# Optimization experiments

Measured on AMD Instinct MI355X. Metric: run time of the kernel, lower is better.

## Reference

```python
import jax, jax.numpy as jnp
import numpy as np

B, N, E, D, M, T, P, HS, HN, C, NH = 64, 1024, 512, 1024, 16, 12, 2048, 2048, 64, 4, 8
EPS = 1e-8


def _ln(x, g, b):
    m = x.mean(-1, keepdims=True)
    v = ((x - m) ** 2).mean(-1, keepdims=True)
    return (x - m) / jnp.sqrt(v + 1e-5) * g + b


def _glu(x):
    a, b = jnp.split(x, 2, axis=-1)
    return a * jax.nn.sigmoid(b)


def setup_inputs() -> dict:
    key = jax.random.key(0)
    ks = jax.random.split(key, 24)
    s = 0.02
    rn = lambda k, sh: jax.random.normal(k, sh, jnp.float32) * s
    inp = {
        'kv_tokens': jax.random.normal(ks[0], (B, N, E), jnp.float32),
        'raw_r_act': jnp.full((P,), -10.0, jnp.float32),  # no_decay_init
        'raw_r_out': jnp.full((P,), -10.0, jnp.float32),
        'q_w': rn(ks[1], (E, P)), 'q_b': jnp.zeros((E,), jnp.float32),
        'in_proj_w': rn(ks[2], (3 * E, E)), 'in_proj_b': jnp.zeros((3 * E,), jnp.float32),
        'out_proj_w': rn(ks[3], (E, E)), 'out_proj_b': jnp.zeros((E,), jnp.float32),
        'z_ln_g': jnp.ones((D,), jnp.float32), 'z_ln_b': jnp.zeros((D,), jnp.float32),
        'o_ln_g': jnp.ones((E,), jnp.float32), 'o_ln_b': jnp.zeros((E,), jnp.float32),
        'gate_w': rn(ks[4], (D, D + E)), 'gate_b': jnp.zeros((D,), jnp.float32),
        'cand_w': rn(ks[5], (D, D + E)), 'cand_b': jnp.zeros((D,), jnp.float32),
        'syn1_w': rn(ks[6], (HS, D + E)), 'syn1_b': jnp.zeros((HS,), jnp.float32),
        'syn2_w': rn(ks[7], (D, HS)), 'syn2_b': jnp.zeros((D,), jnp.float32),
        'nlm1_w': rn(ks[8], (D, M, 2 * HN)), 'nlm1_b': jnp.zeros((D, 2 * HN), jnp.float32),
        'nlm2_w': rn(ks[9], (D, HN, 2)), 'nlm2_b': jnp.zeros((D, 2), jnp.float32),
        'head_w': rn(ks[10], (C, P)), 'head_b': jnp.zeros((C,), jnp.float32),
        'act_left': jax.random.randint(ks[11], (P,), 0, D),
        'act_right': jax.random.randint(ks[12], (P,), 0, D),
        'out_left': jax.random.randint(ks[13], (P,), 0, D),
        'out_right': jax.random.randint(ks[14], (P,), 0, D),
    }
    return inp


def reference(kv_tokens, raw_r_act, raw_r_out, q_w, q_b, in_proj_w, in_proj_b,
              out_proj_w, out_proj_b, z_ln_g, z_ln_b, o_ln_g, o_ln_b,
              gate_w, gate_b, cand_w, cand_b, syn1_w, syn1_b, syn2_w, syn2_b,
              nlm1_w, nlm1_b, nlm2_w, nlm2_b, head_w, head_b,
              act_left, act_right, out_left, out_right):
    dh = E // NH
    scale = 1.0 / np.sqrt(dh).astype(np.float32)
    Wq, Wk, Wv = jnp.split(in_proj_w, 3, axis=0)
    bq, bk, bv = jnp.split(in_proj_b, 3, axis=0)
    # K/V are tick-invariant: project once.
    k = (kv_tokens @ Wk.T + bk).reshape(B, N, NH, dh).transpose(0, 2, 1, 3)  # [B,H,N,dh]
    v = (kv_tokens @ Wv.T + bv).reshape(B, N, NH, dh).transpose(0, 2, 1, 3)
    decay_a = jnp.exp(-jax.nn.softplus(raw_r_act))[None, :]
    decay_o = jnp.exp(-jax.nn.softplus(raw_r_out))[None, :]

    z0 = jnp.zeros((B, D), kv_tokens.dtype)
    A0 = jnp.zeros((B, D, M), kv_tokens.dtype)
    # init_state with z0 == 0 -> alpha 0, beta 1, synch 0
    a_a0 = z0[:, act_left] * z0[:, act_right]
    b_a0 = jnp.ones_like(a_a0)
    s_a0 = a_a0 / jnp.sqrt(b_a0 + EPS)
    a_o0 = z0[:, out_left] * z0[:, out_right]
    b_o0 = jnp.ones_like(a_o0)

    def tick(carry, _):
        z, A, a_a, b_a, s_a, a_o, b_o = carry
        # attention query from action sync
        q = s_a @ q_w.T + q_b                                  # [B,E]
        qh = (q @ Wq.T + bq).reshape(B, NH, 1, dh)
        scores = jnp.einsum('bhqd,bhnd->bhqn', qh, k) * scale  # [B,H,1,N]
        attn = jax.nn.softmax(scores, axis=-1)
        o = jnp.einsum('bhqn,bhnd->bhqd', attn, v).reshape(B, E)
        o = o @ out_proj_w.T + out_proj_b
        o = _ln(o, o_ln_g, o_ln_b)                             # LN on o
        zn = _ln(z, z_ln_g, z_ln_b)                            # LN on z
        # gated fusion
        u = jnp.concatenate([zn, o], axis=-1)
        g = jax.nn.sigmoid(u @ gate_w.T + gate_b)
        h = jnp.tanh(u @ cand_w.T + cand_b)
        z_bar = (1.0 - g) * zn + g * h
        fused = jnp.concatenate([z_bar, o], axis=-1)           # [B,D+E]
        # synapse MLP -> pre-activation
        pre = jax.nn.gelu(fused @ syn1_w.T + syn1_b, approximate=False) @ syn2_w.T + syn2_b
        A = jnp.concatenate([A[:, :, 1:], pre[:, :, None]], axis=-1)  # shift history
        # deep NLM (per-neuron SuperLinear + GLU, twice)
        h1 = _glu(jnp.einsum('bdm,dmh->bdh', A, nlm1_w) + nlm1_b)
        z = _glu(jnp.einsum('bdh,dho->bdo', h1, nlm2_w) + nlm2_b)[..., 0]
        # decayed pair synchronisation updates
        a_a = decay_a * a_a + z[:, act_left] * z[:, act_right]
        b_a = decay_a * b_a + 1.0
        s_a = a_a / jnp.sqrt(b_a + EPS)
        a_o = decay_o * a_o + z[:, out_left] * z[:, out_right]
        b_o = decay_o * b_o + 1.0
        s_o = a_o / jnp.sqrt(b_o + EPS)
        logits = s_o @ head_w.T + head_b                       # [B,C]
        return (z, A, a_a, b_a, s_a, a_o, b_o), (logits, z)

    carry0 = (z0, A0, a_a0, b_a0, s_a0, a_o0, b_o0)
    _, (logits_t, z_t) = jax.lax.scan(tick, carry0, None, length=T)
    logits_ticks = jnp.transpose(logits_t, (1, 2, 0))          # [B,C,T]
    p = jnp.clip(jax.nn.softmax(logits_ticks, axis=1), 1e-8, None)
    ent = -(p * jnp.log(p)).sum(axis=1)
    certainty = 1.0 - ent / np.float32(np.log(C))              # [B,T]
    z_ticks = jnp.transpose(z_t, (1, 0, 2))                    # [B,T,D]
    return logits_ticks, certainty, z_ticks
```

## Files before the change

### kernel.cpp

```cpp
#include <hip/hip_runtime.h>
#include <hip/hip_bf16.h>

#define B_ 64
#define N_ 1024
#define E_ 512
#define D_ 1024
#define M_ 16
#define T_ 12
#define P_ 2048
#define HS_ 2048
#define HN_ 64
#define C_ 4
#define NH_ 8
#define DH_ 64

typedef __attribute__((ext_vector_type(8))) short bf16x8;
typedef __attribute__((ext_vector_type(4))) float f32x4;

__device__ __forceinline__ float bf2f(unsigned int u) {
    union { unsigned int i; float f; } c; c.i = (u & 0xffffu) << 16; return c.f;
}
__device__ __forceinline__ unsigned short f2bf(float f) {
    union { float f; unsigned int i; } c; c.f = f;
    unsigned int x = c.i;
    unsigned int r = x + 0x7fffu + ((x >> 16) & 1u);
    return (unsigned short)(r >> 16);
}

__global__ void init_kernel(unsigned short* s_a_bf, float* a_a, float* b_a, float* a_o, float* b_o, float* z) {
    int i = blockIdx.x * 256 + threadIdx.x;
    if (i < B_ * P_) { a_a[i] = 0.f; b_a[i] = 1.f; a_o[i] = 0.f; b_o[i] = 1.f; s_a_bf[i] = 0; }
    if (i < B_ * D_) z[i] = 0.f;
}

__global__ __launch_bounds__(256) void cvt_bf16_kernel(const float* __restrict__ in,
                                                       unsigned short* __restrict__ out, int n4) {
    int i = blockIdx.x * 256 + threadIdx.x;
    if (i < n4) {
        float4 v = ((const float4*)in)[i];
        ushort4 o;
        o.x = f2bf(v.x); o.y = f2bf(v.y); o.z = f2bf(v.z); o.w = f2bf(v.w);
        ((ushort4*)out)[i] = o;
    }
}

__global__ __launch_bounds__(256) void cvt_ilv_kernel(const float* __restrict__ g,
                                                      const float* __restrict__ c,
                                                      unsigned short* __restrict__ out) {
    int r = blockIdx.x;
    const float* src = (r & 1) ? (c + (size_t)(r >> 1) * 1536) : (g + (size_t)(r >> 1) * 1536);
    for (int k = threadIdx.x * 4; k < 1536; k += 1024) {
        float4 v = *(const float4*)(src + k);
        ushort4 o;
        o.x = f2bf(v.x); o.y = f2bf(v.y); o.z = f2bf(v.z); o.w = f2bf(v.w);
        *(ushort4*)(out + (size_t)r * 1536 + k) = o;
    }
}

__global__ __launch_bounds__(256) void transpose_cvt_kernel(const float* __restrict__ in,
                                                            unsigned short* __restrict__ out,
                                                            int R, int Ccols) {
    __shared__ float tb[32][33];
    int c0 = blockIdx.x * 32, r0 = blockIdx.y * 32;
    int tx = threadIdx.x & 31, ty = threadIdx.x >> 5;
#pragma unroll
    for (int i = 0; i < 32; i += 8) tb[ty + i][tx] = in[(size_t)(r0 + ty + i) * Ccols + c0 + tx];
    __syncthreads();
#pragma unroll
    for (int i = 0; i < 32; i += 8) out[(size_t)(c0 + ty + i) * R + r0 + tx] = f2bf(tb[tx][ty + i]);
}

__global__ __launch_bounds__(256) void bcomb_kernel(const float* __restrict__ in_proj_w,
                                                    const float* __restrict__ in_proj_b,
                                                    const float* __restrict__ q_b,
                                                    float* __restrict__ bc) {
    int e = blockIdx.x * 256 + threadIdx.x;
    if (e < E_) {
        const float* wr = in_proj_w + (size_t)e * E_;
        float s = in_proj_b[e];
        for (int k = 0; k < E_; k += 4) {
            float4 w4 = *(const float4*)(wr + k);
            float4 q4 = *(const float4*)(q_b + k);
            s += w4.x * q4.x + w4.y * q4.y + w4.z * q4.z + w4.w * q4.w;
        }
        bc[e] = s;
    }
}

__global__ __launch_bounds__(256) void br_kernel(const float* __restrict__ in_proj_w,
                                                 const float* __restrict__ bc,
                                                 float* __restrict__ br) {
    int g = blockIdx.x * 256 + threadIdx.x;
    int h = g >> 9, j = g & 511;
    const float* Wk = in_proj_w + (size_t)E_ * E_;
    float s = 0.f;
    for (int e = 0; e < 64; e++) {
        s += Wk[(size_t)(h * 64 + e) * E_ + j] * bc[h * 64 + e];
    }
    br[g] = s;
}

template <bool HAS_BIAS>
__global__ __launch_bounds__(256) void gemm_bt_kernel(const unsigned short* __restrict__ A,
                                                      const unsigned short* __restrict__ Bt,
                                                      const float* __restrict__ bias,
                                                      unsigned short* __restrict__ C,
                                                      int M, int N, int K) {
    __shared__ __align__(16) unsigned short ldsA[2][4096];
    __shared__ __align__(16) unsigned short ldsB[2][4096];
    int id = blockIdx.y * gridDim.x + blockIdx.x;
    int nwg = gridDim.x * gridDim.y;
    int swz = (id & 7) * (nwg >> 3) + (id >> 3);
    int bx = swz % gridDim.x, by = swz / gridDim.x;
    int m0 = by * 128;
    int n0 = bx * 128;
    int tid = threadIdx.x;
    int wv = tid >> 6, l = tid & 63;
    int wr = wv >> 1, wc = wv & 1;
    int lr = l & 15, lg = l >> 4;
    f32x4 acc[4][4] = {};

    auto stage = [&](int buf, int kt) {
        int k0 = kt * 32;
#pragma unroll
        for (int i = 0; i < 2; i++) {
            int tsk = tid + 256 * i;
            int r = tsk >> 2, g = tsk & 3;
            int gs = (g ^ (r & 3)) * 8;
            __builtin_amdgcn_global_load_lds(
                (const __attribute__((address_space(1))) void*)(A + (size_t)(m0 + r) * K + k0 + gs),
                (__attribute__((address_space(3))) void*)&ldsA[buf][tsk * 8], 16, 0, 0);
        }
#pragma unroll
        for (int i = 0; i < 2; i++) {
            int tsk = tid + 256 * i;
            int r = tsk >> 2, g = tsk & 3;
            int gs = (g ^ (r & 3)) * 8;
            __builtin_amdgcn_global_load_lds(
                (const __attribute__((address_space(1))) void*)(Bt + (size_t)(n0 + r) * K + k0 + gs),
                (__attribute__((address_space(3))) void*)&ldsB[buf][tsk * 8], 16, 0, 0);
        }
    };

    int nt = K >> 5;
    stage(0, 0);
    for (int t = 0; t < nt; t++) {
        int cur = t & 1;
        if (t + 1 < nt) {
            stage(cur ^ 1, t + 1);
            asm volatile("s_waitcnt vmcnt(4)" ::: "memory");
        } else {
            asm volatile("s_waitcnt vmcnt(0)" ::: "memory");
        }
        __builtin_amdgcn_s_barrier();
        bf16x8 af[4], bfr[4];
#pragma unroll
        for (int mi = 0; mi < 4; mi++) {
            int r = wr * 64 + mi * 16 + lr;
            af[mi] = *(const bf16x8*)&ldsA[cur][r * 32 + ((lg ^ (r & 3)) << 3)];
        }
#pragma unroll
        for (int ni = 0; ni < 4; ni++) {
            int c = wc * 64 + ni * 16 + lr;
            bfr[ni] = *(const bf16x8*)&ldsB[cur][c * 32 + ((lg ^ (c & 3)) << 3)];
        }
#pragma unroll
        for (int mi = 0; mi < 4; mi++)
#pragma unroll
            for (int ni = 0; ni < 4; ni++)
                acc[mi][ni] = __builtin_amdgcn_mfma_f32_16x16x32_bf16(af[mi], bfr[ni], acc[mi][ni], 0, 0, 0);
        __builtin_amdgcn_s_barrier();
    }
#pragma unroll
    for (int ni = 0; ni < 4; ni++) {
        int col = n0 + wc * 64 + ni * 16 + lr;
        float bv = HAS_BIAS ? bias[col] : 0.0f;
#pragma unroll
        for (int mi = 0; mi < 4; mi++) {
            int row = m0 + wr * 64 + mi * 16 + lg * 4;
#pragma unroll
            for (int r = 0; r < 4; r++) {
                C[(size_t)(row + r) * N + col] = f2bf(acc[mi][ni][r] + bv);
            }
        }
    }
}

__global__ __launch_bounds__(256) void gemm_hb_kernel(const unsigned short* __restrict__ A0, int lda, size_t sAz,
                                                      const unsigned short* __restrict__ B0, int ldb, size_t sBz,
                                                      unsigned short* __restrict__ C0, int ldc, size_t sCz,
                                                      int K) {
    __shared__ __align__(16) unsigned short ldsA[2][4096];
    __shared__ __align__(16) unsigned short ldsB[2][4096];
    const unsigned short* A = A0 + blockIdx.z * sAz;
    const unsigned short* Bt = B0 + blockIdx.z * sBz;
    unsigned short* C = C0 + blockIdx.z * sCz;
    int m0 = blockIdx.y * 128, n0 = blockIdx.x * 128;
    int tid = threadIdx.x;
    int wv = tid >> 6, l = tid & 63;
    int wr = wv >> 1, wc = wv & 1;
    int lr = l & 15, lg = l >> 4;
    f32x4 acc[4][4] = {};

    auto stage = [&](int buf, int kt) {
        int k0 = kt * 32;
#pragma unroll
        for (int i = 0; i < 2; i++) {
            int tsk = tid + 256 * i;
            int r = tsk >> 2, g = tsk & 3;
            int gs = (g ^ (r & 3)) * 8;
            __builtin_amdgcn_global_load_lds(
                (const __attribute__((address_space(1))) void*)(A + (size_t)(m0 + r) * lda + k0 + gs),
                (__attribute__((address_space(3))) void*)&ldsA[buf][tsk * 8], 16, 0, 0);
        }
#pragma unroll
        for (int i = 0; i < 2; i++) {
            int tsk = tid + 256 * i;
            int r = tsk >> 2, g = tsk & 3;
            int gs = (g ^ (r & 3)) * 8;
            __builtin_amdgcn_global_load_lds(
                (const __attribute__((address_space(1))) void*)(Bt + (size_t)(n0 + r) * ldb + k0 + gs),
                (__attribute__((address_space(3))) void*)&ldsB[buf][tsk * 8], 16, 0, 0);
        }
    };

    int nt = K >> 5;
    stage(0, 0);
    for (int t = 0; t < nt; t++) {
        int cur = t & 1;
        if (t + 1 < nt) {
            stage(cur ^ 1, t + 1);
            asm volatile("s_waitcnt vmcnt(4)" ::: "memory");
        } else {
            asm volatile("s_waitcnt vmcnt(0)" ::: "memory");
        }
        __builtin_amdgcn_s_barrier();
        bf16x8 af[4], bfr[4];
#pragma unroll
        for (int mi = 0; mi < 4; mi++) {
            int r = wr * 64 + mi * 16 + lr;
            af[mi] = *(const bf16x8*)&ldsA[cur][r * 32 + ((lg ^ (r & 3)) << 3)];
        }
#pragma unroll
        for (int ni = 0; ni < 4; ni++) {
            int c = wc * 64 + ni * 16 + lr;
            bfr[ni] = *(const bf16x8*)&ldsB[cur][c * 32 + ((lg ^ (c & 3)) << 3)];
        }
#pragma unroll
        for (int mi = 0; mi < 4; mi++)
#pragma unroll
            for (int ni = 0; ni < 4; ni++)
                acc[mi][ni] = __builtin_amdgcn_mfma_f32_16x16x32_bf16(af[mi], bfr[ni], acc[mi][ni], 0, 0, 0);
        __builtin_amdgcn_s_barrier();
    }
#pragma unroll
    for (int ni = 0; ni < 4; ni++) {
        int col = n0 + wc * 64 + ni * 16 + lr;
#pragma unroll
        for (int mi = 0; mi < 4; mi++) {
            int row = m0 + wr * 64 + mi * 16 + lg * 4;
#pragma unroll
            for (int r = 0; r < 4; r++) {
                C[(size_t)(row + r) * ldc + col] = f2bf(acc[mi][ni][r]);
            }
        }
    }
}

template <int EPI>
__global__ __launch_bounds__(256) void gemmNK_kernel(const unsigned short* __restrict__ A,
                                                     const unsigned short* __restrict__ W,
                                                     const float* __restrict__ bias0,
                                                     const float* __restrict__ bias1,
                                                     const float* __restrict__ zn32,
                                                     void* __restrict__ outp,
                                                     int N, int K) {
    __shared__ __align__(16) unsigned short ldsA[4][2][2048];
    __shared__ __align__(16) unsigned short ldsB[4][2][512];
    int n0 = blockIdx.x * 16;
    int tid = threadIdx.x;
    int w = tid >> 6, l = tid & 63;
    int Kw = K >> 2;
    int kb = w * Kw;
    int lr = l & 15, lg = l >> 4;
    int ar = l >> 2, ag = l & 3;
    f32x4 acc[4] = {};

    auto stage = [&](int buf, int kt) {
        int k0 = kb + (kt << 5);
#pragma unroll
        for (int i = 0; i < 4; i++) {
            int row = i * 16 + ar;
            int gs = (ag ^ (row & 3)) << 3;
            __builtin_amdgcn_global_load_lds(
                (const __attribute__((address_space(1))) void*)(A + (size_t)row * K + k0 + gs),
                (__attribute__((address_space(3))) void*)&ldsA[w][buf][i * 512 + l * 8], 16, 0, 0);
        }
        {
            int col = ar;
            int gs = (ag ^ (col & 3)) << 3;
            __builtin_amdgcn_global_load_lds(
                (const __attribute__((address_space(1))) void*)(W + (size_t)(n0 + col) * K + k0 + gs),
                (__attribute__((address_space(3))) void*)&ldsB[w][buf][l * 8], 16, 0, 0);
        }
    };

    int nt = Kw >> 5;
    stage(0, 0);
    for (int t = 0; t < nt; t++) {
        int cur = t & 1;
        if (t + 1 < nt) {
            stage(cur ^ 1, t + 1);
            asm volatile("s_waitcnt vmcnt(5)" ::: "memory");
        } else {
            asm volatile("s_waitcnt vmcnt(0)" ::: "memory");
        }
        bf16x8 bf = *(const bf16x8*)&ldsB[w][cur][lr * 32 + ((lg ^ (lr & 3)) << 3)];
#pragma unroll
        for (int mi = 0; mi < 4; mi++) {
            int rr = mi * 16 + lr;
            bf16x8 af = *(const bf16x8*)&ldsA[w][cur][rr * 32 + ((lg ^ (rr & 3)) << 3)];
            acc[mi] = __builtin_amdgcn_mfma_f32_16x16x32_bf16(af, bf, acc[mi], 0, 0, 0);
        }
    }
    __syncthreads();
    float* red = (float*)&ldsA[0][0][0];
#pragma unroll
    for (int mi = 0; mi < 4; mi++) {
        int row = mi * 16 + lg * 4;
#pragma unroll
        for (int q = 0; q < 4; q++) red[w * 1024 + (row + q) * 16 + lr] = acc[mi][q];
    }
    __syncthreads();
    int b = tid >> 2, c4 = (tid & 3) << 2;
    f32x4 s = *(f32x4*)&red[b * 16 + c4];
#pragma unroll
    for (int ww = 1; ww < 4; ww++) {
        f32x4 v = *(f32x4*)&red[ww * 1024 + b * 16 + c4];
        s[0] += v[0]; s[1] += v[1]; s[2] += v[2]; s[3] += v[3];
    }
    int col = n0 + c4;
    if (EPI == 0) {
        unsigned short* out = (unsigned short*)outp;
        ushort4 o;
        o.x = f2bf(0.125f * (s[0] + bias0[col + 0]));
        o.y = f2bf(0.125f * (s[1] + bias0[col + 1]));
        o.z = f2bf(0.125f * (s[2] + bias0[col + 2]));
        o.w = f2bf(0.125f * (s[3] + bias0[col + 3]));
        *(ushort4*)(out + (size_t)b * N + col) = o;
    } else if (EPI == 1) {
        float* out = (float*)outp;
        *(f32x4*)(out + (size_t)b * N + col) = s;
    } else if (EPI == 2) {
        unsigned short* out = (unsigned short*)outp;
        int j0 = col >> 1;
#pragma unroll
        for (int pp = 0; pp < 2; pp++) {
            int j = j0 + pp;
            float g = 1.0f / (1.0f + expf(-(s[pp * 2] + bias0[j])));
            float h = tanhf(s[pp * 2 + 1] + bias1[j]);
            float zb = (1.0f - g) * zn32[(size_t)b * D_ + j] + g * h;
            out[(size_t)b * 1536 + j] = f2bf(zb);
        }
    } else if (EPI == 3) {
        unsigned short* out = (unsigned short*)outp;
        ushort4 o;
#pragma unroll
        for (int j = 0; j < 4; j++) {
            float pre = s[j] + bias0[col + j];
            float val = 0.5f * pre * (1.0f + erff(pre * 0.70710678118654752f));
            ((unsigned short*)&o)[j] = f2bf(val);
        }
        *(ushort4*)(out + (size_t)b * N + col) = o;
    } else {
        float* out = (float*)outp;
#pragma unroll
        for (int j = 0; j < 4; j++) {
            out[(size_t)(col + j) * 64 + b] = s[j] + bias0[col + j];
        }
    }
}

__global__ __launch_bounds__(256) void scoreX_kernel(const unsigned short* __restrict__ X,
                                                     const unsigned short* __restrict__ r_bf,
                                                     float* __restrict__ S) {
    int b = blockIdx.y;
    int n0 = blockIdx.x * 128;
    int tid = threadIdx.x;
    int wv = tid >> 6, l = tid & 63;
    int lr = l & 15, lg = l >> 4;
    const unsigned short* Xb = X + ((size_t)b * 1024 + n0) * 512;
    const unsigned short* rb = r_bf + (size_t)b * 4096 + (size_t)(lr & 7) * 512 + lg * 8;
    f32x4 acc[2] = {};
#pragma unroll
    for (int kt = 0; kt < 16; kt++) {
        int k0 = kt * 32;
        bf16x8 bfrag = *(const bf16x8*)(rb + k0);
#pragma unroll
        for (int mi = 0; mi < 2; mi++) {
            int row = (wv * 2 + mi) * 16 + lr;
            bf16x8 afrag = *(const bf16x8*)(Xb + (size_t)row * 512 + k0 + lg * 8);
            acc[mi] = __builtin_amdgcn_mfma_f32_16x16x32_bf16(afrag, bfrag, acc[mi], 0, 0, 0);
        }
    }
    if (lr < 8) {
#pragma unroll
        for (int mi = 0; mi < 2; mi++) {
            int rowbase = (wv * 2 + mi) * 16 + lg * 4;
#pragma unroll
            for (int q = 0; q < 4; q++) {
                S[((size_t)b * 8 + lr) * 1024 + n0 + rowbase + q] = acc[mi][q];
            }
        }
    }
}

__global__ __launch_bounds__(256) void attnV_kernel(const float* __restrict__ S,
                                                    const unsigned short* __restrict__ vbuf,
                                                    unsigned short* __restrict__ o_bf) {
    int bh = blockIdx.x;
    int b = bh >> 3, h = bh & 7;
    __shared__ float sc[N_];
    __shared__ float red[8];
    __shared__ float opart[4][DH_];
    int tid = threadIdx.x;
    int w = tid >> 6, lane = tid & 63;
    const float* Ss = S + ((size_t)b * 8 + h) * 1024;
    float myv[4];
#pragma unroll
    for (int i = 0; i < 4; i++) myv[i] = Ss[tid + i * 256];
    float m = fmaxf(fmaxf(myv[0], myv[1]), fmaxf(myv[2], myv[3]));
#pragma unroll
    for (int off = 32; off >= 1; off >>= 1) m = fmaxf(m, __shfl_xor(m, off, 64));
    if (lane == 0) red[w] = m;
    __syncthreads();
    m = fmaxf(fmaxf(red[0], red[1]), fmaxf(red[2], red[3]));
    float s = 0.f;
#pragma unroll
    for (int i = 0; i < 4; i++) {
        float e = expf(myv[i] - m);
        sc[tid + i * 256] = e;
        s += e;
    }
#pragma unroll
    for (int off = 32; off >= 1; off >>= 1) s += __shfl_xor(s, off, 64);
    if (lane == 0) red[4 + w] = s;
    __syncthreads();
    float inv = 1.0f / (red[4] + red[5] + red[6] + red[7]);
    const unsigned short* vb = vbuf + (size_t)b * 1024 * 512 + h * DH_;
    int ng = lane >> 4, d4 = (lane & 15) << 2;
    float a0 = 0.f, a1 = 0.f, a2 = 0.f, a3 = 0.f;
    int n0 = w * 256;
    for (int i = 0; i < 64; i++) {
        int n = n0 + i * 4 + ng;
        uint2 pv = *(const uint2*)(vb + (size_t)n * 512 + d4);
        float sv = sc[n];
        a0 += sv * bf2f(pv.x);
        a1 += sv * bf2f(pv.x >> 16);
        a2 += sv * bf2f(pv.y);
        a3 += sv * bf2f(pv.y >> 16);
    }
    a0 += __shfl_xor(a0, 16, 64); a0 += __shfl_xor(a0, 32, 64);
    a1 += __shfl_xor(a1, 16, 64); a1 += __shfl_xor(a1, 32, 64);
    a2 += __shfl_xor(a2, 16, 64); a2 += __shfl_xor(a2, 32, 64);
    a3 += __shfl_xor(a3, 16, 64); a3 += __shfl_xor(a3, 32, 64);
    if (lane < 16) {
        opart[w][d4 + 0] = a0;
        opart[w][d4 + 1] = a1;
        opart[w][d4 + 2] = a2;
        opart[w][d4 + 3] = a3;
    }
    __syncthreads();
    if (tid < DH_) {
        float r = (opart[0][tid] + opart[1][tid] + opart[2][tid] + opart[3][tid]) * inv;
        o_bf[(size_t)b * E_ + h * DH_ + tid] = f2bf(r);
    }
}

__global__ __launch_bounds__(256) void reduce_oln_kernel(const float* __restrict__ opre,
                                                         const float* __restrict__ bout,
                                                         const float* __restrict__ og,
                                                         const float* __restrict__ obv,
                                                         const float* __restrict__ z,
                                                         const float* __restrict__ zg,
                                                         const float* __restrict__ zbv,
                                                         unsigned short* __restrict__ u_bf,
                                                         unsigned short* __restrict__ fused_bf,
                                                         float* __restrict__ zn32) {
    int b = blockIdx.x, tid = threadIdx.x;
    __shared__ float red[16];
    float v[2];
#pragma unroll
    for (int i = 0; i < 2; i++) {
        int e = tid + i * 256;
        v[i] = opre[(size_t)b * E_ + e] + bout[e];
    }
    int w = tid >> 6, lane = tid & 63;
    float s1 = v[0] + v[1];
    float s2 = v[0] * v[0] + v[1] * v[1];
#pragma unroll
    for (int off = 32; off >= 1; off >>= 1) { s1 += __shfl_xor(s1, off, 64); s2 += __shfl_xor(s2, off, 64); }
    if (lane == 0) { red[w] = s1; red[4 + w] = s2; }
    __syncthreads();
    s1 = red[0] + red[1] + red[2] + red[3];
    s2 = red[4] + red[5] + red[6] + red[7];
    float mean = s1 * (1.0f / 512.0f);
    float var = s2 * (1.0f / 512.0f) - mean * mean;
    float rstd = 1.0f / sqrtf(var + 1e-5f);
#pragma unroll
    for (int i = 0; i < 2; i++) {
        int e = tid + i * 256;
        unsigned short val = f2bf((v[i] - mean) * rstd * og[e] + obv[e]);
        u_bf[(size_t)b * 1536 + D_ + e] = val;
        fused_bf[(size_t)b * 1536 + D_ + e] = val;
    }
    float zl[4];
    float t1 = 0.f, t2 = 0.f;
#pragma unroll
    for (int i = 0; i < 4; i++) {
        int d = tid + i * 256;
        zl[i] = z[(size_t)b * D_ + d];
        t1 += zl[i]; t2 += zl[i] * zl[i];
    }
#pragma unroll
    for (int off = 32; off >= 1; off >>= 1) { t1 += __shfl_xor(t1, off, 64); t2 += __shfl_xor(t2, off, 64); }
    __syncthreads();
    if (lane == 0) { red[8 + w] = t1; red[12 + w] = t2; }
    __syncthreads();
    t1 = red[8] + red[9] + red[10] + red[11];
    t2 = red[12] + red[13] + red[14] + red[15];
    float zmean = t1 * (1.0f / 1024.0f);
    float zvar = t2 * (1.0f / 1024.0f) - zmean * zmean;
    float zr = 1.0f / sqrtf(zvar + 1e-5f);
#pragma unroll
    for (int i = 0; i < 4; i++) {
        int d = tid + i * 256;
        float zn = (zl[i] - zmean) * zr * zg[d] + zbv[d];
        u_bf[(size_t)b * 1536 + d] = f2bf(zn);
        zn32[(size_t)b * D_ + d] = zn;
    }
}

template <int NT>
__global__ __launch_bounds__(256) void nlm_kernel(const float* __restrict__ AbufT,
                                                  const unsigned short* __restrict__ w1g_bf,
                                                  const float* __restrict__ b1g,
                                                  const float* __restrict__ w2g,
                                                  const float* __restrict__ b2g,
                                                  float* __restrict__ z,
                                                  float* __restrict__ zt) {
    __shared__ float w1s[4][2048];
    __shared__ float b1s[4][128];
    __shared__ float w2s[4][128];
    __shared__ float b2s[4][2];
    int tid = threadIdx.x;
    int w = tid >> 6, lane = tid & 63;
    int d = blockIdx.x * 4 + w;
    for (int i = lane * 2; i < 2048; i += 128) {
        unsigned int pk = *(const unsigned int*)(w1g_bf + (size_t)d * 2048 + i);
        w1s[w][i] = bf2f(pk);
        w1s[w][i + 1] = bf2f(pk >> 16);
    }
    for (int i = lane; i < 128; i += 64) {
        b1s[w][i] = b1g[(size_t)d * 128 + i];
        w2s[w][i] = w2g[(size_t)d * 128 + i];
    }
    if (lane < 2) b2s[w][lane] = b2g[d * 2 + lane];
    __syncthreads();
    const int b = lane;
    float av[NT];
#pragma unroll
    for (int s = 0; s < NT; s++) av[s] = AbufT[((size_t)s * D_ + d) * 64 + b];
    constexpr int moff = M_ - NT;
    float o0 = b2s[w][0], o1 = b2s[w][1];
    for (int hh = 0; hh < 64; hh++) {
        float a = b1s[w][hh], bb = b1s[w][hh + 64];
#pragma unroll
        for (int s = 0; s < NT; s++) {
            float x = av[s];
            a += x * w1s[w][(s + moff) * 128 + hh];
            bb += x * w1s[w][(s + moff) * 128 + hh + 64];
        }
        float z1 = a / (1.0f + expf(-bb));
        o0 += z1 * w2s[w][hh * 2];
        o1 += z1 * w2s[w][hh * 2 + 1];
    }
    float zv = o0 / (1.0f + expf(-o1));
    z[(size_t)b * D_ + d] = zv;
    zt[((size_t)b * T_ + (NT - 1)) * D_ + d] = zv;
}

__global__ __launch_bounds__(256) void synchead_kernel(const float* __restrict__ z,
                                                       const int* __restrict__ act_l, const int* __restrict__ act_r,
                                                       const int* __restrict__ out_l, const int* __restrict__ out_r,
                                                       const float* __restrict__ raw_a, const float* __restrict__ raw_o,
                                                       const float* __restrict__ head_w, const float* __restrict__ head_b,
                                                       float* __restrict__ a_a, float* __restrict__ b_a,
                                                       unsigned short* __restrict__ s_a_bf,
                                                       float* __restrict__ a_o, float* __restrict__ b_o,
                                                       float* __restrict__ out_logits, float* __restrict__ out_cert, int t) {
    int b = blockIdx.x, tid = threadIdx.x;
    __shared__ float zv[D_];
    __shared__ float red[4][4];
    for (int i = tid; i < D_; i += 256) zv[i] = z[(size_t)b * D_ + i];
    __syncthreads();
    float l0 = 0.f, l1 = 0.f, l2 = 0.f, l3 = 0.f;
    for (int p = tid; p < P_; p += 256) {
        size_t ip = (size_t)b * P_ + p;
        float zl = zv[act_l[p]], zr = zv[act_r[p]];
        float da = 1.0f / (1.0f + expf(raw_a[p]));
        float aa = da * a_a[ip] + zl * zr;
        float ba = da * b_a[ip] + 1.0f;
        a_a[ip] = aa; b_a[ip] = ba;
        s_a_bf[(size_t)b * P_ + p] = f2bf(aa / sqrtf(ba + 1e-8f));
        float zlo = zv[out_l[p]], zro = zv[out_r[p]];
        float dz = 1.0f / (1.0f + expf(raw_o[p]));
        float ao = dz * a_o[ip] + zlo * zro;
        float bo = dz * b_o[ip] + 1.0f;
        a_o[ip] = ao; b_o[ip] = bo;
        float so = ao / sqrtf(bo + 1e-8f);
        l0 += so * head_w[p];
        l1 += so * head_w[P_ + p];
        l2 += so * head_w[2 * P_ + p];
        l3 += so * head_w[3 * P_ + p];
    }
    int w = tid >> 6, lane = tid & 63;
#pragma unroll
    for (int off = 32; off >= 1; off >>= 1) {
        l0 += __shfl_xor(l0, off, 64);
        l1 += __shfl_xor(l1, off, 64);
        l2 += __shfl_xor(l2, off, 64);
        l3 += __shfl_xor(l3, off, 64);
    }
    if (lane == 0) { red[w][0] = l0; red[w][1] = l1; red[w][2] = l2; red[w][3] = l3; }
    __syncthreads();
    if (tid == 0) {
        float lg[4];
#pragma unroll
        for (int c = 0; c < 4; c++) {
            lg[c] = red[0][c] + red[1][c] + red[2][c] + red[3][c] + head_b[c];
            out_logits[((size_t)b * C_ + c) * T_ + t] = lg[c];
        }
        float m = fmaxf(fmaxf(lg[0], lg[1]), fmaxf(lg[2], lg[3]));
        float e0 = expf(lg[0] - m), e1 = expf(lg[1] - m), e2 = expf(lg[2] - m), e3 = expf(lg[3] - m);
        float inv = 1.0f / (e0 + e1 + e2 + e3);
        float ent = 0.f, pp;
        pp = fmaxf(e0 * inv, 1e-8f); ent -= pp * logf(pp);
        pp = fmaxf(e1 * inv, 1e-8f); ent -= pp * logf(pp);
        pp = fmaxf(e2 * inv, 1e-8f); ent -= pp * logf(pp);
        pp = fmaxf(e3 * inv, 1e-8f); ent -= pp * logf(pp);
        out_cert[(size_t)b * T_ + t] = 1.0f - ent * (1.0f / 1.3862943611198906f);
    }
}

extern "C" void kernel_launch(void* const* d_in, const int* in_sizes, int n_in,
                              void* d_out, int out_size, void* d_ws, size_t ws_size,
                              hipStream_t stream) {
    const float* kv_tokens  = (const float*)d_in[0];
    const float* raw_r_act  = (const float*)d_in[1];
    const float* raw_r_out  = (const float*)d_in[2];
    const float* q_w        = (const float*)d_in[3];
    const float* q_b        = (const float*)d_in[4];
    const float* in_proj_w  = (const float*)d_in[5];
    const float* in_proj_b  = (const float*)d_in[6];
    const float* out_proj_w = (const float*)d_in[7];
    const float* out_proj_b = (const float*)d_in[8];
    const float* z_ln_g     = (const float*)d_in[9];
    const float* z_ln_b     = (const float*)d_in[10];
    const float* o_ln_g     = (const float*)d_in[11];
    const float* o_ln_b     = (const float*)d_in[12];
    const float* gate_w     = (const float*)d_in[13];
    const float* gate_b     = (const float*)d_in[14];
    const float* cand_w     = (const float*)d_in[15];
    const float* cand_b     = (const float*)d_in[16];
    const float* syn1_w     = (const float*)d_in[17];
    const float* syn1_b     = (const float*)d_in[18];
    const float* syn2_w     = (const float*)d_in[19];
    const float* syn2_b     = (const float*)d_in[20];
    const float* nlm1_w     = (const float*)d_in[21];
    const float* nlm1_b     = (const float*)d_in[22];
    const float* nlm2_w     = (const float*)d_in[23];
    const float* nlm2_b     = (const float*)d_in[24];
    const float* head_w     = (const float*)d_in[25];
    const float* head_b     = (const float*)d_in[26];
    const int* act_l        = (const int*)d_in[27];
    const int* act_r        = (const int*)d_in[28];
    const int* out_l        = (const int*)d_in[29];
    const int* out_r        = (const int*)d_in[30];

    float* out = (float*)d_out;
    float* out_logits = out;
    float* out_cert = out + B_ * C_ * T_;
    float* out_zt = out_cert + B_ * T_;

    char* ws = (char*)d_ws;
    size_t off = 0;
    auto alloc = [&](size_t bytes) { void* p = ws + off; off += (bytes + 255) & ~(size_t)255; return p; };
    unsigned short* kv_bf   = (unsigned short*)alloc((size_t)B_ * N_ * E_ * 2);
    unsigned short* vbuf    = (unsigned short*)alloc((size_t)B_ * N_ * E_ * 2);
    unsigned short* Wv_bf   = (unsigned short*)alloc((size_t)E_ * E_ * 2);
    unsigned short* Wq_bf   = (unsigned short*)alloc((size_t)E_ * E_ * 2);
    unsigned short* WkT_bf  = (unsigned short*)alloc((size_t)E_ * E_ * 2);
    unsigned short* qwT_bf  = (unsigned short*)alloc((size_t)P_ * E_ * 2);
    unsigned short* WcT_bf  = (unsigned short*)alloc((size_t)P_ * E_ * 2);
    unsigned short* Gmat    = (unsigned short*)alloc((size_t)4096 * P_ * 2);
    unsigned short* Wgc_bf  = (unsigned short*)alloc((size_t)2048 * 1536 * 2);
    unsigned short* Ws1_bf  = (unsigned short*)alloc((size_t)2048 * 1536 * 2);
    unsigned short* Ws2_bf  = (unsigned short*)alloc((size_t)1024 * 2048 * 2);
    unsigned short* Wout_bf = (unsigned short*)alloc((size_t)E_ * E_ * 2);
    unsigned short* nlm1w_bf= (unsigned short*)alloc((size_t)1024 * 2048 * 2);
    float* bc   = (float*)alloc(E_ * 4);
    float* brv  = (float*)alloc(4096 * 4);
    unsigned short* s_a_bf  = (unsigned short*)alloc((size_t)B_ * P_ * 2);
    unsigned short* r_bf    = (unsigned short*)alloc((size_t)B_ * 4096 * 2);
    float* Sbuf = (float*)alloc((size_t)B_ * 8 * N_ * 4);
    unsigned short* o_bf    = (unsigned short*)alloc((size_t)B_ * E_ * 2);
    unsigned short* u_bf    = (unsigned short*)alloc((size_t)B_ * 1536 * 2);
    unsigned short* fused_bf= (unsigned short*)alloc((size_t)B_ * 1536 * 2);
    unsigned short* tbuf_bf = (unsigned short*)alloc((size_t)B_ * HS_ * 2);
    float* opre = (float*)alloc((size_t)B_ * E_ * 4);
    float* zn32 = (float*)alloc((size_t)B_ * D_ * 4);
    float* a_a  = (float*)alloc((size_t)B_ * P_ * 4);
    float* b_a  = (float*)alloc((size_t)B_ * P_ * 4);
    float* a_o  = (float*)alloc((size_t)B_ * P_ * 4);
    float* b_o  = (float*)alloc((size_t)B_ * P_ * 4);
    float* zbuf = (float*)alloc((size_t)B_ * D_ * 4);
    float* AbufT = (float*)alloc((size_t)T_ * D_ * B_ * 4);

    init_kernel<<<512, 256, 0, stream>>>(s_a_bf, a_a, b_a, a_o, b_o, zbuf);

    cvt_bf16_kernel<<<(B_ * N_ * E_ / 4) / 256, 256, 0, stream>>>(kv_tokens, kv_bf, B_ * N_ * E_ / 4);
    cvt_bf16_kernel<<<256, 256, 0, stream>>>(in_proj_w + (size_t)2 * E_ * E_, Wv_bf, E_ * E_ / 4);
    cvt_bf16_kernel<<<256, 256, 0, stream>>>(in_proj_w, Wq_bf, E_ * E_ / 4);
    transpose_cvt_kernel<<<dim3(16, 16), 256, 0, stream>>>(in_proj_w + (size_t)E_ * E_, WkT_bf, E_, E_);
    transpose_cvt_kernel<<<dim3(P_ / 32, E_ / 32), 256, 0, stream>>>(q_w, qwT_bf, E_, P_);
    bcomb_kernel<<<2, 256, 0, stream>>>(in_proj_w, in_proj_b, q_b, bc);
    br_kernel<<<16, 256, 0, stream>>>(in_proj_w, bc, brv);
    gemm_bt_kernel<false><<<dim3(E_ / 128, P_ / 128), 256, 0, stream>>>(qwT_bf, Wq_bf, nullptr, WcT_bf, P_, E_, E_);
    gemm_hb_kernel<<<dim3(P_ / 128, E_ / 128, NH_), 256, 0, stream>>>(WkT_bf, E_, 64,
                                                                      WcT_bf, E_, 64,
                                                                      Gmat, P_, (size_t)512 * P_, 64);
    cvt_ilv_kernel<<<2048, 256, 0, stream>>>(gate_w, cand_w, Wgc_bf);
    cvt_bf16_kernel<<<(2048 * 1536 / 4 + 255) / 256, 256, 0, stream>>>(syn1_w, Ws1_bf, 2048 * 1536 / 4);
    cvt_bf16_kernel<<<(1024 * 2048 / 4 + 255) / 256, 256, 0, stream>>>(syn2_w, Ws2_bf, 1024 * 2048 / 4);
    cvt_bf16_kernel<<<(1024 * 2048 / 4 + 255) / 256, 256, 0, stream>>>(nlm1_w, nlm1w_bf, 1024 * 2048 / 4);
    cvt_bf16_kernel<<<256, 256, 0, stream>>>(out_proj_w, Wout_bf, E_ * E_ / 4);
    gemm_bt_kernel<true><<<dim3(E_ / 128, B_ * N_ / 128), 256, 0, stream>>>(kv_bf, Wv_bf, in_proj_b + 2 * E_,
                                                                            vbuf, B_ * N_, E_, E_);

    for (int t = 0; t < T_; t++) {
        gemmNK_kernel<0><<<256, 256, 0, stream>>>(s_a_bf, Gmat, brv, nullptr, nullptr, r_bf, 4096, P_);
        scoreX_kernel<<<dim3(8, 64), 256, 0, stream>>>(kv_bf, r_bf, Sbuf);
        attnV_kernel<<<B_ * NH_, 256, 0, stream>>>(Sbuf, vbuf, o_bf);
        gemmNK_kernel<1><<<32, 256, 0, stream>>>(o_bf, Wout_bf, nullptr, nullptr, nullptr, opre, E_, E_);
        reduce_oln_kernel<<<64, 256, 0, stream>>>(opre, out_proj_b, o_ln_g, o_ln_b,
                                                  zbuf, z_ln_g, z_ln_b, u_bf, fused_bf, zn32);
        gemmNK_kernel<2><<<128, 256, 0, stream>>>(u_bf, Wgc_bf, gate_b, cand_b, zn32, fused_bf, 2048, 1536);
        gemmNK_kernel<3><<<128, 256, 0, stream>>>(fused_bf, Ws1_bf, syn1_b, nullptr, nullptr, tbuf_bf, 2048, 1536);
        gemmNK_kernel<4><<<64, 256, 0, stream>>>(tbuf_bf, Ws2_bf, syn2_b, nullptr, nullptr,
                                                 AbufT + (size_t)t * D_ * 64, 1024, 2048);
        switch (t) {
            case 0:  nlm_kernel<1><<<256, 256, 0, stream>>>(AbufT, nlm1w_bf, nlm1_b, nlm2_w, nlm2_b, zbuf, out_zt); break;
            case 1:  nlm_kernel<2><<<256, 256, 0, stream>>>(AbufT, nlm1w_bf, nlm1_b, nlm2_w, nlm2_b, zbuf, out_zt); break;
            case 2:  nlm_kernel<3><<<256, 256, 0, stream>>>(AbufT, nlm1w_bf, nlm1_b, nlm2_w, nlm2_b, zbuf, out_zt); break;
            case 3:  nlm_kernel<4><<<256, 256, 0, stream>>>(AbufT, nlm1w_bf, nlm1_b, nlm2_w, nlm2_b, zbuf, out_zt); break;
            case 4:  nlm_kernel<5><<<256, 256, 0, stream>>>(AbufT, nlm1w_bf, nlm1_b, nlm2_w, nlm2_b, zbuf, out_zt); break;
            case 5:  nlm_kernel<6><<<256, 256, 0, stream>>>(AbufT, nlm1w_bf, nlm1_b, nlm2_w, nlm2_b, zbuf, out_zt); break;
            case 6:  nlm_kernel<7><<<256, 256, 0, stream>>>(AbufT, nlm1w_bf, nlm1_b, nlm2_w, nlm2_b, zbuf, out_zt); break;
            case 7:  nlm_kernel<8><<<256, 256, 0, stream>>>(AbufT, nlm1w_bf, nlm1_b, nlm2_w, nlm2_b, zbuf, out_zt); break;
            case 8:  nlm_kernel<9><<<256, 256, 0, stream>>>(AbufT, nlm1w_bf, nlm1_b, nlm2_w, nlm2_b, zbuf, out_zt); break;
            case 9:  nlm_kernel<10><<<256, 256, 0, stream>>>(AbufT, nlm1w_bf, nlm1_b, nlm2_w, nlm2_b, zbuf, out_zt); break;
            case 10: nlm_kernel<11><<<256, 256, 0, stream>>>(AbufT, nlm1w_bf, nlm1_b, nlm2_w, nlm2_b, zbuf, out_zt); break;
            default: nlm_kernel<12><<<256, 256, 0, stream>>>(AbufT, nlm1w_bf, nlm1_b, nlm2_w, nlm2_b, zbuf, out_zt); break;
        }
        synchead_kernel<<<64, 256, 0, stream>>>(zbuf, act_l, act_r, out_l, out_r, raw_r_act, raw_r_out,
                                                head_w, head_b, a_a, b_a, s_a_bf, a_o, b_o,
                                                out_logits, out_cert, t);
    }
}
```

Measured before the change: 1.340 ms.

## Fuse score and attention-V kernels, precompute decay normalizers, batch weight conversions

Merges the score and softmax·V kernels into one per-batch kernel that keeps scores in shared memory, which removes the global S buffer round trip and one launch per tick. The per-batch b_a/b_o recurrences are replaced by a per-pair table of 1/sqrt(b) over ticks computed once, along with the decay factors. Several bf16 weight conversions are merged into one grid-stride kernel. The fused attention kernel runs only 64 blocks on a GPU with many compute units, so it loses parallelism relative to the previous 512-block and 512-block launches.

```diff
diff --git a/kernel.cpp b/kernel.cpp
--- a/kernel.cpp
+++ b/kernel.cpp
@@ -27,10 +27,29 @@
     return (unsigned short)(r >> 16);
 }
 
-__global__ void init_kernel(unsigned short* s_a_bf, float* a_a, float* b_a, float* a_o, float* b_o, float* z) {
+__global__ void init_kernel(unsigned short* s_a_bf, float* a_a, float* a_o, float* z) {
     int i = blockIdx.x * 256 + threadIdx.x;
-    if (i < B_ * P_) { a_a[i] = 0.f; b_a[i] = 1.f; a_o[i] = 0.f; b_o[i] = 1.f; s_a_bf[i] = 0; }
+    if (i < B_ * P_) { a_a[i] = 0.f; a_o[i] = 0.f; s_a_bf[i] = 0; }
     if (i < B_ * D_) z[i] = 0.f;
+}
+
+__global__ __launch_bounds__(256) void decay_prep_kernel(const float* __restrict__ raw_a,
+                                                         const float* __restrict__ raw_o,
+                                                         float* __restrict__ da, float* __restrict__ dz,
+                                                         float* __restrict__ invsa, float* __restrict__ invso) {
+    int p = blockIdx.x * 256 + threadIdx.x;
+    if (p < P_) {
+        float a = 1.f / (1.f + expf(raw_a[p]));
+        float o = 1.f / (1.f + expf(raw_o[p]));
+        da[p] = a; dz[p] = o;
+        float ba = 1.f, bo = 1.f;
+        for (int t = 0; t < T_; t++) {
+            ba = a * ba + 1.f;
+            bo = o * bo + 1.f;
+            invsa[t * P_ + p] = 1.0f / sqrtf(ba + 1e-8f);
+            invso[t * P_ + p] = 1.0f / sqrtf(bo + 1e-8f);
+        }
+    }
 }
 
 __global__ __launch_bounds__(256) void cvt_bf16_kernel(const float* __restrict__ in,
@@ -41,6 +60,33 @@
         ushort4 o;
         o.x = f2bf(v.x); o.y = f2bf(v.y); o.z = f2bf(v.z); o.w = f2bf(v.w);
         ((ushort4*)out)[i] = o;
+    }
+}
+
+__global__ __launch_bounds__(256) void cvt_all_kernel(
+    const float* s0, unsigned short* d0, int n0,
+    const float* s1, unsigned short* d1, int n1,
+    const float* s2, unsigned short* d2, int n2,
+    const float* s3, unsigned short* d3, int n3,
+    const float* s4, unsigned short* d4, int n4,
+    const float* s5, unsigned short* d5, int n5) {
+    int total = n0 + n1 + n2 + n3 + n4 + n5;
+    for (int i = blockIdx.x * 256 + threadIdx.x; i < total; i += gridDim.x * 256) {
+        const float* s; unsigned short* d; int j = i;
+        if (j < n0) { s = s0; d = d0; }
+        else { j -= n0;
+        if (j < n1) { s = s1; d = d1; }
+        else { j -= n1;
+        if (j < n2) { s = s2; d = d2; }
+        else { j -= n2;
+        if (j < n3) { s = s3; d = d3; }
+        else { j -= n3;
+        if (j < n4) { s = s4; d = d4; }
+        else { j -= n4; s = s5; d = d5; } } } } }
+        float4 v = ((const float4*)s)[j];
+        ushort4 o;
+        o.x = f2bf(v.x); o.y = f2bf(v.y); o.z = f2bf(v.z); o.w = f2bf(v.w);
+        ((ushort4*)d)[j] = o;
     }
 }
 
@@ -381,99 +427,98 @@
     }
 }
 
-__global__ __launch_bounds__(256) void scoreX_kernel(const unsigned short* __restrict__ X,
-                                                     const unsigned short* __restrict__ r_bf,
-                                                     float* __restrict__ S) {
-    int b = blockIdx.y;
-    int n0 = blockIdx.x * 128;
+__global__ __launch_bounds__(256) void attn_kernel(const unsigned short* __restrict__ X,
+                                                   const unsigned short* __restrict__ r_bf,
+                                                   const unsigned short* __restrict__ vbuf,
+                                                   unsigned short* __restrict__ o_bf) {
+    __shared__ float S[8][1028];
+    __shared__ float opart[4][8][68];
+    __shared__ float inv[8];
+    int b = blockIdx.x;
     int tid = threadIdx.x;
     int wv = tid >> 6, l = tid & 63;
     int lr = l & 15, lg = l >> 4;
-    const unsigned short* Xb = X + ((size_t)b * 1024 + n0) * 512;
+    const unsigned short* Xb = X + (size_t)b * 1024 * 512;
     const unsigned short* rb = r_bf + (size_t)b * 4096 + (size_t)(lr & 7) * 512 + lg * 8;
-    f32x4 acc[2] = {};
-#pragma unroll
-    for (int kt = 0; kt < 16; kt++) {
-        int k0 = kt * 32;
-        bf16x8 bfrag = *(const bf16x8*)(rb + k0);
-#pragma unroll
-        for (int mi = 0; mi < 2; mi++) {
-            int row = (wv * 2 + mi) * 16 + lr;
-            bf16x8 afrag = *(const bf16x8*)(Xb + (size_t)row * 512 + k0 + lg * 8);
-            acc[mi] = __builtin_amdgcn_mfma_f32_16x16x32_bf16(afrag, bfrag, acc[mi], 0, 0, 0);
-        }
-    }
-    if (lr < 8) {
-#pragma unroll
-        for (int mi = 0; mi < 2; mi++) {
-            int rowbase = (wv * 2 + mi) * 16 + lg * 4;
-#pragma unroll
-            for (int q = 0; q < 4; q++) {
-                S[((size_t)b * 8 + lr) * 1024 + n0 + rowbase + q] = acc[mi][q];
+    for (int nt8 = 0; nt8 < 8; nt8++) {
+        int nbase = nt8 * 128;
+        f32x4 acc[2] = {};
+#pragma unroll
+        for (int kt = 0; kt < 16; kt++) {
+            int k0 = kt * 32;
+            bf16x8 bfrag = *(const bf16x8*)(rb + k0);
+#pragma unroll
+            for (int mi = 0; mi < 2; mi++) {
+                int row = nbase + (wv * 2 + mi) * 16 + lr;
+                bf16x8 afrag = *(const bf16x8*)(Xb + (size_t)row * 512 + k0 + lg * 8);
+                acc[mi] = __builtin_amdgcn_mfma_f32_16x16x32_bf16(afrag, bfrag, acc[mi], 0, 0, 0);
             }
         }
-    }
-}
-
-__global__ __launch_bounds__(256) void attnV_kernel(const float* __restrict__ S,
-                                                    const unsigned short* __restrict__ vbuf,
-                                                    unsigned short* __restrict__ o_bf) {
-    int bh = blockIdx.x;
-    int b = bh >> 3, h = bh & 7;
-    __shared__ float sc[N_];
-    __shared__ float red[8];
-    __shared__ float opart[4][DH_];
-    int tid = threadIdx.x;
-    int w = tid >> 6, lane = tid & 63;
-    const float* Ss = S + ((size_t)b * 8 + h) * 1024;
-    float myv[4];
-#pragma unroll
-    for (int i = 0; i < 4; i++) myv[i] = Ss[tid + i * 256];
-    float m = fmaxf(fmaxf(myv[0], myv[1]), fmaxf(myv[2], myv[3]));
-#pragma unroll
-    for (int off = 32; off >= 1; off >>= 1) m = fmaxf(m, __shfl_xor(m, off, 64));
-    if (lane == 0) red[w] = m;
-    __syncthreads();
-    m = fmaxf(fmaxf(red[0], red[1]), fmaxf(red[2], red[3]));
-    float s = 0.f;
-#pragma unroll
-    for (int i = 0; i < 4; i++) {
-        float e = expf(myv[i] - m);
-        sc[tid + i * 256] = e;
-        s += e;
-    }
-#pragma unroll
-    for (int off = 32; off >= 1; off >>= 1) s += __shfl_xor(s, off, 64);
-    if (lane == 0) red[4 + w] = s;
-    __syncthreads();
-    float inv = 1.0f / (red[4] + red[5] + red[6] + red[7]);
-    const unsigned short* vb = vbuf + (size_t)b * 1024 * 512 + h * DH_;
-    int ng = lane >> 4, d4 = (lane & 15) << 2;
-    float a0 = 0.f, a1 = 0.f, a2 = 0.f, a3 = 0.f;
-    int n0 = w * 256;
-    for (int i = 0; i < 64; i++) {
-        int n = n0 + i * 4 + ng;
-        uint2 pv = *(const uint2*)(vb + (size_t)n * 512 + d4);
-        float sv = sc[n];
-        a0 += sv * bf2f(pv.x);
-        a1 += sv * bf2f(pv.x >> 16);
-        a2 += sv * bf2f(pv.y);
-        a3 += sv * bf2f(pv.y >> 16);
-    }
-    a0 += __shfl_xor(a0, 16, 64); a0 += __shfl_xor(a0, 32, 64);
-    a1 += __shfl_xor(a1, 16, 64); a1 += __shfl_xor(a1, 32, 64);
-    a2 += __shfl_xor(a2, 16, 64); a2 += __shfl_xor(a2, 32, 64);
-    a3 += __shfl_xor(a3, 16, 64); a3 += __shfl_xor(a3, 32, 64);
-    if (lane < 16) {
-        opart[w][d4 + 0] = a0;
-        opart[w][d4 + 1] = a1;
-        opart[w][d4 + 2] = a2;
-        opart[w][d4 + 3] = a3;
-    }
-    __syncthreads();
-    if (tid < DH_) {
-        float r = (opart[0][tid] + opart[1][tid] + opart[2][tid] + opart[3][tid]) * inv;
-        o_bf[(size_t)b * E_ + h * DH_ + tid] = f2bf(r);
+        if (lr < 8) {
+#pragma unroll
+            for (int mi = 0; mi < 2; mi++) {
+                int rowbase = nbase + (wv * 2 + mi) * 16 + lg * 4;
+#pragma unroll
+                for (int q = 0; q < 4; q++) S[lr][rowbase + q] = acc[mi][q];
+            }
+        }
+    }
+    __syncthreads();
+#pragma unroll
+    for (int rep = 0; rep < 2; rep++) {
+        int h = wv * 2 + rep;
+        float vals[16];
+        float m = -1e30f;
+#pragma unroll
+        for (int i = 0; i < 16; i++) { vals[i] = S[h][l + i * 64]; m = fmaxf(m, vals[i]); }
+#pragma unroll
+        for (int off = 32; off >= 1; off >>= 1) m = fmaxf(m, __shfl_xor(m, off, 64));
+        float s = 0.f;
+#pragma unroll
+        for (int i = 0; i < 16; i++) {
+            float e = expf(vals[i] - m);
+            S[h][l + i * 64] = e;
+            s += e;
+        }
+#pragma unroll
+        for (int off = 32; off >= 1; off >>= 1) s += __shfl_xor(s, off, 64);
+        if (l == 0) inv[h] = 1.0f / s;
+    }
+    __syncthreads();
+    const unsigned short* vb = vbuf + (size_t)b * 1024 * 512;
+    int ng = l >> 4, d4 = (l & 15) << 2;
+    int n0 = wv * 256;
+    for (int h = 0; h < 8; h++) {
+        const float* Sh = S[h];
+        const unsigned short* vbh = vb + h * 64;
+        float a0 = 0.f, a1 = 0.f, a2 = 0.f, a3 = 0.f;
+        for (int i = 0; i < 64; i++) {
+            int n = n0 + i * 4 + ng;
+            uint2 pv = *(const uint2*)(vbh + (size_t)n * 512 + d4);
+            float sv = Sh[n];
+            a0 += sv * bf2f(pv.x);
+            a1 += sv * bf2f(pv.x >> 16);
+            a2 += sv * bf2f(pv.y);
+            a3 += sv * bf2f(pv.y >> 16);
+        }
+        a0 += __shfl_xor(a0, 16, 64); a0 += __shfl_xor(a0, 32, 64);
+        a1 += __shfl_xor(a1, 16, 64); a1 += __shfl_xor(a1, 32, 64);
+        a2 += __shfl_xor(a2, 16, 64); a2 += __shfl_xor(a2, 32, 64);
+        a3 += __shfl_xor(a3, 16, 64); a3 += __shfl_xor(a3, 32, 64);
+        if (l < 16) {
+            opart[wv][h][d4 + 0] = a0;
+            opart[wv][h][d4 + 1] = a1;
+            opart[wv][h][d4 + 2] = a2;
+            opart[wv][h][d4 + 3] = a3;
+        }
+    }
+    __syncthreads();
+#pragma unroll
+    for (int rep = 0; rep < 2; rep++) {
+        int e = tid + rep * 256;
+        int h = e >> 6, d = e & 63;
+        float r = (opart[0][h][d] + opart[1][h][d] + opart[2][h][d] + opart[3][h][d]) * inv[h];
+        o_bf[(size_t)b * E_ + e] = f2bf(r);
     }
 }
 
@@ -593,11 +638,12 @@
 __global__ __launch_bounds__(256) void synchead_kernel(const float* __restrict__ z,
                                                        const int* __restrict__ act_l, const int* __restrict__ act_r,
                                                        const int* __restrict__ out_l, const int* __restrict__ out_r,
-                                                       const float* __restrict__ raw_a, const float* __restrict__ raw_o,
+                                                       const float* __restrict__ da, const float* __restrict__ dz,
+                                                       const float* __restrict__ invsa_t, const float* __restrict__ invso_t,
                                                        const float* __restrict__ head_w, const float* __restrict__ head_b,
-                                                       float* __restrict__ a_a, float* __restrict__ b_a,
+                                                       float* __restrict__ a_a,
                                                        unsigned short* __restrict__ s_a_bf,
-                                                       float* __restrict__ a_o, float* __restrict__ b_o,
+                                                       float* __restrict__ a_o,
                                                        float* __restrict__ out_logits, float* __restrict__ out_cert, int t) {
     int b = blockIdx.x, tid = threadIdx.x;
     __shared__ float zv[D_];
@@ -607,18 +653,12 @@
     float l0 = 0.f, l1 = 0.f, l2 = 0.f, l3 = 0.f;
     for (int p = tid; p < P_; p += 256) {
         size_t ip = (size_t)b * P_ + p;
-        float zl = zv[act_l[p]], zr = zv[act_r[p]];
-        float da = 1.0f / (1.0f + expf(raw_a[p]));
-        float aa = da * a_a[ip] + zl * zr;
-        float ba = da * b_a[ip] + 1.0f;
-        a_a[ip] = aa; b_a[ip] = ba;
-        s_a_bf[(size_t)b * P_ + p] = f2bf(aa / sqrtf(ba + 1e-8f));
-        float zlo = zv[out_l[p]], zro = zv[out_r[p]];
-        float dz = 1.0f / (1.0f + expf(raw_o[p]));
-        float ao = dz * a_o[ip] + zlo * zro;
-        float bo = dz * b_o[ip] + 1.0f;
-        a_o[ip] = ao; b_o[ip] = bo;
-        float so = ao / sqrtf(bo + 1e-8f);
+        float aa = da[p] * a_a[ip] + zv[act_l[p]] * zv[act_r[p]];
+        a_a[ip] = aa;
+        s_a_bf[(size_t)b * P_ + p] = f2bf(aa * invsa_t[p]);
+        float ao = dz[p] * a_o[ip] + zv[out_l[p]] * zv[out_r[p]];
+        a_o[ip] = ao;
+        float so = ao * invso_t[p];
         l0 += so * head_w[p];
         l1 += so * head_w[P_ + p];
         l2 += so * head_w[2 * P_ + p];
@@ -711,9 +751,12 @@
     unsigned short* nlm1w_bf= (unsigned short*)alloc((size_t)1024 * 2048 * 2);
     float* bc   = (float*)alloc(E_ * 4);
     float* brv  = (float*)alloc(4096 * 4);
+    float* da   = (float*)alloc(P_ * 4);
+    float* dzv  = (float*)alloc(P_ * 4);
+    float* invsa = (float*)alloc((size_t)T_ * P_ * 4);
+    float* invso = (float*)alloc((size_t)T_ * P_ * 4);
     unsigned short* s_a_bf  = (unsigned short*)alloc((size_t)B_ * P_ * 2);
     unsigned short* r_bf    = (unsigned short*)alloc((size_t)B_ * 4096 * 2);
-    float* Sbuf = (float*)alloc((size_t)B_ * 8 * N_ * 4);
     unsigned short* o_bf    = (unsigned short*)alloc((size_t)B_ * E_ * 2);
     unsigned short* u_bf    = (unsigned short*)alloc((size_t)B_ * 1536 * 2);
     unsigned short* fused_bf= (unsigned short*)alloc((size_t)B_ * 1536 * 2);
@@ -721,17 +764,22 @@
     float* opre = (float*)alloc((size_t)B_ * E_ * 4);
     float* zn32 = (float*)alloc((size_t)B_ * D_ * 4);
     float* a_a  = (float*)alloc((size_t)B_ * P_ * 4);
-    float* b_a  = (float*)alloc((size_t)B_ * P_ * 4);
     float* a_o  = (float*)alloc((size_t)B_ * P_ * 4);
-    float* b_o  = (float*)alloc((size_t)B_ * P_ * 4);
     float* zbuf = (float*)alloc((size_t)B_ * D_ * 4);
     float* AbufT = (float*)alloc((size_t)T_ * D_ * B_ * 4);
 
-    init_kernel<<<512, 256, 0, stream>>>(s_a_bf, a_a, b_a, a_o, b_o, zbuf);
+    init_kernel<<<512, 256, 0, stream>>>(s_a_bf, a_a, a_o, zbuf);
+    decay_prep_kernel<<<8, 256, 0, stream>>>(raw_r_act, raw_r_out, da, dzv, invsa, invso);
 
     cvt_bf16_kernel<<<(B_ * N_ * E_ / 4) / 256, 256, 0, stream>>>(kv_tokens, kv_bf, B_ * N_ * E_ / 4);
-    cvt_bf16_kernel<<<256, 256, 0, stream>>>(in_proj_w + (size_t)2 * E_ * E_, Wv_bf, E_ * E_ / 4);
-    cvt_bf16_kernel<<<256, 256, 0, stream>>>(in_proj_w, Wq_bf, E_ * E_ / 4);
+    cvt_all_kernel<<<2048, 256, 0, stream>>>(
+        in_proj_w + (size_t)2 * E_ * E_, Wv_bf, E_ * E_ / 4,
+        in_proj_w, Wq_bf, E_ * E_ / 4,
+        out_proj_w, Wout_bf, E_ * E_ / 4,
+        syn1_w, Ws1_bf, 2048 * 1536 / 4,
+        syn2_w, Ws2_bf, 1024 * 2048 / 4,
+        nlm1_w, nlm1w_bf, 1024 * 2048 / 4);
+    cvt_ilv_kernel<<<2048, 256, 0, stream>>>(gate_w, cand_w, Wgc_bf);
     transpose_cvt_kernel<<<dim3(16, 16), 256, 0, stream>>>(in_proj_w + (size_t)E_ * E_, WkT_bf, E_, E_);
     transpose_cvt_kernel<<<dim3(P_ / 32, E_ / 32), 256, 0, stream>>>(q_w, qwT_bf, E_, P_);
     bcomb_kernel<<<2, 256, 0, stream>>>(in_proj_w, in_proj_b, q_b, bc);
@@ -740,18 +788,12 @@
     gemm_hb_kernel<<<dim3(P_ / 128, E_ / 128, NH_), 256, 0, stream>>>(WkT_bf, E_, 64,
                                                                       WcT_bf, E_, 64,
                                                                       Gmat, P_, (size_t)512 * P_, 64);
-    cvt_ilv_kernel<<<2048, 256, 0, stream>>>(gate_w, cand_w, Wgc_bf);
-    cvt_bf16_kernel<<<(2048 * 1536 / 4 + 255) / 256, 256, 0, stream>>>(syn1_w, Ws1_bf, 2048 * 1536 / 4);
-    cvt_bf16_kernel<<<(1024 * 2048 / 4 + 255) / 256, 256, 0, stream>>>(syn2_w, Ws2_bf, 1024 * 2048 / 4);
-    cvt_bf16_kernel<<<(1024 * 2048 / 4 + 255) / 256, 256, 0, stream>>>(nlm1_w, nlm1w_bf, 1024 * 2048 / 4);
-    cvt_bf16_kernel<<<256, 256, 0, stream>>>(out_proj_w, Wout_bf, E_ * E_ / 4);
     gemm_bt_kernel<true><<<dim3(E_ / 128, B_ * N_ / 128), 256, 0, stream>>>(kv_bf, Wv_bf, in_proj_b + 2 * E_,
                                                                             vbuf, B_ * N_, E_, E_);
 
     for (int t = 0; t < T_; t++) {
         gemmNK_kernel<0><<<256, 256, 0, stream>>>(s_a_bf, Gmat, brv, nullptr, nullptr, r_bf, 4096, P_);
-        scoreX_kernel<<<dim3(8, 64), 256, 0, stream>>>(kv_bf, r_bf, Sbuf);
-        attnV_kernel<<<B_ * NH_, 256, 0, stream>>>(Sbuf, vbuf, o_bf);
+        attn_kernel<<<64, 256, 0, stream>>>(kv_bf, r_bf, vbuf, o_bf);
         gemmNK_kernel<1><<<32, 256, 0, stream>>>(o_bf, Wout_bf, nullptr, nullptr, nullptr, opre, E_, E_);
         reduce_oln_kernel<<<64, 256, 0, stream>>>(opre, out_proj_b, o_ln_g, o_ln_b,
                                                   zbuf, z_ln_g, z_ln_b, u_bf, fused_bf, zn32);
@@ -773,8 +815,9 @@
             case 10: nlm_kernel<11><<<256, 256, 0, stream>>>(AbufT, nlm1w_bf, nlm1_b, nlm2_w, nlm2_b, zbuf, out_zt); break;
             default: nlm_kernel<12><<<256, 256, 0, stream>>>(AbufT, nlm1w_bf, nlm1_b, nlm2_w, nlm2_b, zbuf, out_zt); break;
         }
-        synchead_kernel<<<64, 256, 0, stream>>>(zbuf, act_l, act_r, out_l, out_r, raw_r_act, raw_r_out,
-                                                head_w, head_b, a_a, b_a, s_a_bf, a_o, b_o,
+        synchead_kernel<<<64, 256, 0, stream>>>(zbuf, act_l, act_r, out_l, out_r, da, dzv,
+                                                invsa + t * P_, invso + t * P_,
+                                                head_w, head_b, a_a, s_a_bf, a_o,
                                                 out_logits, out_cert, t);
     }
 }
```

Measured after the change: 2.053 ms. +53.2%, slower.
